# Kernel tuning notes

Measured on AMD Instinct MI355X. Metric: run time of the kernel, lower is better.

## Reference

```python
import jax, jax.numpy as jnp
import numpy as np

FIELD_DIMS = [26000] * 39
EMBED_DIM = 16
MLP_DIMS = [1024, 512, 256]
BATCH = 16384
EPS = 1e-5
OFFSETS = jnp.asarray(np.concatenate(([0], np.cumsum(FIELD_DIMS)[:-1])), dtype=jnp.int64)


def _bn_fields(x, g, b):
    # BatchNorm1d(num_fields) on (B, F, E): stats over (batch, embed) per field (training-mode batch stats)
    mu = x.mean(axis=(0, 2), keepdims=True)
    var = x.var(axis=(0, 2), keepdims=True)
    return (x - mu) / jnp.sqrt(var + EPS) * g[None, :, None] + b[None, :, None]


def _bn1d(x, g, b):
    # BatchNorm1d on (B, D): stats over batch
    mu = x.mean(axis=0)
    var = x.var(axis=0)
    return (x - mu) / jnp.sqrt(var + EPS) * g + b


def setup_inputs() -> dict:
    key = jax.random.key(0)
    ks = jax.random.split(key, 16)
    V = sum(FIELD_DIMS)
    F = len(FIELD_DIMS)
    E = EMBED_DIM
    D = F * E  # 624
    init = lambda k, shape, s: (jax.random.normal(k, shape) * s).astype(jnp.float32)
    inp = {}
    inp["x"] = jax.random.randint(ks[0], (BATCH, F), 0, FIELD_DIMS[0], dtype=jnp.int64)
    inp["emb_table"] = init(ks[1], (V, E), 0.01)
    inp["lin_table"] = init(ks[2], (V, 1), 0.01)
    inp["lin_bias"] = jnp.zeros((1,), jnp.float32)
    inp["bn_g"] = jnp.ones((F,), jnp.float32)
    inp["bn_b"] = jnp.zeros((F,), jnp.float32)
    inp["ctrl_w"] = init(ks[3], (D, F), D ** -0.5)
    inp["ctrl_b"] = jnp.zeros((F,), jnp.float32)
    inp["ctrl_bn_g"] = jnp.ones((F,), jnp.float32)
    inp["ctrl_bn_b"] = jnp.zeros((F,), jnp.float32)
    dims = [D] + MLP_DIMS
    for i in range(3):
        inp[f"w{i+1}"] = init(ks[4 + i], (dims[i], dims[i + 1]), dims[i] ** -0.5)
        inp[f"b{i+1}"] = jnp.zeros((dims[i + 1],), jnp.float32)
        inp[f"g{i+1}"] = jnp.ones((dims[i + 1],), jnp.float32)
        inp[f"be{i+1}"] = jnp.zeros((dims[i + 1],), jnp.float32)
    inp["w_out"] = init(ks[7], (dims[-1], 1), dims[-1] ** -0.5)
    inp["b_out"] = jnp.zeros((1,), jnp.float32)
    inp["k"] = 20
    return inp


def reference(x, emb_table, lin_table, lin_bias, bn_g, bn_b,
              ctrl_w, ctrl_b, ctrl_bn_g, ctrl_bn_b,
              w1, b1, g1, be1, w2, b2, g2, be2, w3, b3, g3, be3,
              w_out, b_out, k):
    B, F = x.shape
    idx = x + OFFSETS[None, :]                      # (B, F) global vocab ids
    embed = emb_table[idx]                          # (B, F, E) gather
    embed = _bn_fields(embed, bn_g, bn_b)
    flat = embed.reshape(B, -1)                     # (B, F*E)
    # controller MLP: Linear -> BN -> ReLU (dropout inactive at inference)
    weight = jax.nn.relu(_bn1d(flat @ ctrl_w + ctrl_b, ctrl_bn_g, ctrl_bn_b))  # (B, F)
    # kmax_pooling along dim 1: topk values, indices sorted ascending
    kvals, kidx = jax.lax.top_k(weight, k)          # (B, k)
    order = jnp.argsort(kidx, axis=1)
    kidx = jnp.take_along_axis(kidx, order, axis=1)
    kvals = jnp.take_along_axis(kvals, order, axis=1)
    kvals = kvals / jnp.sum(kvals, axis=1, keepdims=True)
    # scatter normalized weights into zero mask
    mask = jnp.zeros((B, F), embed.dtype).at[jnp.arange(B)[:, None], kidx].set(kvals)
    embed = embed * mask[:, :, None]                # elementwise gate
    # wide part: sum of per-field scalar embeddings + bias
    linear = lin_table[idx].sum(axis=1) + lin_bias  # (B, 1)
    # deep part: 3-layer MLP with BN+ReLU, final Linear to 1
    h = embed.reshape(B, -1)
    h = jax.nn.relu(_bn1d(h @ w1 + b1, g1, be1))
    h = jax.nn.relu(_bn1d(h @ w2 + b2, g2, be2))
    h = jax.nn.relu(_bn1d(h @ w3 + b3, g3, be3))
    out = linear + h @ w_out + b_out                # (B, 1)
    return jax.nn.sigmoid(out.squeeze(1))           # (B,)
```

## Files before the change

kernel.cpp:

```cpp
#include <hip/hip_runtime.h>
#include <math.h>
#include <stdint.h>

constexpr int BB = 16384;
constexpr int NF = 39;
constexpr int NE = 16;
constexpr int ND = NF * NE;
constexpr int FIELD_DIM = 26000;
constexpr float EPS_ = 1e-5f;

typedef __bf16 bfx8 __attribute__((ext_vector_type(8)));
typedef float f32x4 __attribute__((ext_vector_type(4)));
typedef short s16x8 __attribute__((ext_vector_type(8)));

static __device__ __forceinline__ unsigned short f2bf(float f) {
    union { float f; unsigned u; } a; a.f = f;
    unsigned r = a.u + 0x7fffu + ((a.u >> 16) & 1u);
    return (unsigned short)(r >> 16);
}
static __device__ __forceinline__ float bf2f(unsigned short u) {
    union { unsigned u; float f; } a; a.u = ((unsigned)u) << 16;
    return a.f;
}

static __device__ __forceinline__ void xcd_map(int l, int lognx, int& bx, int& by) {
    int s = l >> 3;
    bx = s & ((1 << lognx) - 1);
    by = ((l & 7) << 4) + (s >> lognx);
}

__global__ void k_prep(const float* __restrict__ w1, const float* __restrict__ w2,
                       const float* __restrict__ w3, const float* __restrict__ cw,
                       unsigned short* __restrict__ w1t, unsigned short* __restrict__ w2t,
                       unsigned short* __restrict__ w3t, float* __restrict__ wct,
                       double* __restrict__ stats, int nstats) {
    int b = blockIdx.x;
    if (b < 1280) {
        const float* in; unsigned short* outp; int K, N, Kpad, tid;
        if (b < 640)        { in = w1; outp = w1t; K = 624;  N = 1024; Kpad = 640;  tid = b; }
        else if (b < 1152)  { in = w2; outp = w2t; K = 1024; N = 512;  Kpad = 1024; tid = b - 640; }
        else                { in = w3; outp = w3t; K = 512;  N = 256;  Kpad = 512;  tid = b - 1152; }
        int tiles_n = N >> 5;
        int tk = tid / tiles_n, tn = tid % tiles_n;
        __shared__ float tile[32][33];
        int tx = threadIdx.x & 31, ty = threadIdx.x >> 5;
#pragma unroll
        for (int i = 0; i < 4; ++i) {
            int k = tk * 32 + ty + i * 8, n = tn * 32 + tx;
            tile[ty + i * 8][tx] = (k < K) ? in[(size_t)k * N + n] : 0.f;
        }
        __syncthreads();
#pragma unroll
        for (int i = 0; i < 4; ++i) {
            int n = tn * 32 + ty + i * 8, k = tk * 32 + tx;
            outp[(size_t)n * Kpad + k] = f2bf(tile[tx][ty + i * 8]);
        }
    } else if (b < 1397) {
        int gid = (b - 1280) * 256 + threadIdx.x;
        if (gid < 48 * ND) {
            int j = gid / ND, k = gid % ND;
            wct[gid] = (j < NF) ? cw[(size_t)k * NF + j] : 0.f;
        }
    } else {
        int gid = (b - 1397) * 256 + threadIdx.x;
        if (gid < nstats) stats[gid] = 0.0;
    }
}

__global__ void k_field_stats(const int* __restrict__ x, const float* __restrict__ emb,
                              double* __restrict__ stats ) {
    int f = blockIdx.x;
    int r = blockIdx.y * blockDim.x + threadIdx.x;
    double s = 0.0, q = 0.0;
    if (r < BB) {
        long long id = (long long)x[r * NF + f] + (long long)f * FIELD_DIM;
        const float4* p = (const float4*)(emb + id * NE);
#pragma unroll
        for (int i = 0; i < 4; ++i) {
            float4 v = p[i];
            s += (double)v.x; s += (double)v.y; s += (double)v.z; s += (double)v.w;
            q += (double)v.x * v.x; q += (double)v.y * v.y;
            q += (double)v.z * v.z; q += (double)v.w * v.w;
        }
    }
    __shared__ double ls[256], lq[256];
    ls[threadIdx.x] = s; lq[threadIdx.x] = q;
    __syncthreads();
    for (int off = 128; off > 0; off >>= 1) {
        if ((int)threadIdx.x < off) {
            ls[threadIdx.x] += ls[threadIdx.x + off];
            lq[threadIdx.x] += lq[threadIdx.x + off];
        }
        __syncthreads();
    }
    if (threadIdx.x == 0) {
        atomicAdd(&stats[f], ls[0]);
        atomicAdd(&stats[NF + f], lq[0]);
    }
}

__global__ void k_flat_norm(const int* __restrict__ x, const float* __restrict__ emb,
                            const double* __restrict__ stats, const float* __restrict__ bng,
                            const float* __restrict__ bnb, float* __restrict__ flat) {
    __shared__ float sc_s[NF], sh_s[NF];
    if ((int)threadIdx.x < NF) {
        int f = threadIdx.x;
        double cnt = (double)BB * NE;
        double mu = stats[f] / cnt;
        double var = stats[NF + f] / cnt - mu * mu;
        float sc = (float)((double)bng[f] / sqrt(var + (double)EPS_));
        sc_s[f] = sc;
        sh_s[f] = bnb[f] - (float)mu * sc;
    }
    __syncthreads();
    int gid = blockIdx.x * blockDim.x + threadIdx.x;
    if (gid >= BB * NF) return;
    int f = gid % NF;
    long long id = (long long)x[gid] + (long long)f * FIELD_DIM;
    float sc = sc_s[f], sh = sh_s[f];
    const float4* p = (const float4*)(emb + id * NE);
    float4* o = (float4*)(flat) + (size_t)gid * 4;
#pragma unroll
    for (int i = 0; i < 4; ++i) {
        float4 v = p[i];
        o[i] = make_float4(fmaf(v.x, sc, sh), fmaf(v.y, sc, sh),
                           fmaf(v.z, sc, sh), fmaf(v.w, sc, sh));
    }
}

__launch_bounds__(256)
__global__ void k_ctrl_gemm_sk(const float* __restrict__ flat, const float* __restrict__ wct,
                               double* __restrict__ zp) {
    __shared__ float As[64][68];
    __shared__ float Ws[64][49];
    const int t = threadIdx.x;
    const int tn = t & 15;
    const int tm = t >> 4;
    const int bm = blockIdx.x & 255;
    const int half = blockIdx.x >> 8;
    const int m0 = bm * 64;
    const int kbeg = half ? 320 : 0;
    const int kend = half ? 624 : 320;
    double acc[4][3] = {};
    for (int k0 = kbeg; k0 < kend; k0 += 64) {
        const int kl = (kend - k0 >= 64) ? 64 : (kend - k0);
        const int kl4 = kl >> 2;
#pragma unroll
        for (int i = 0; i < 4; ++i) {
            int idx = t + 256 * i;
            int row = idx >> 4, c4 = idx & 15;
            if (c4 < kl4) {
                float4 v = *(const float4*)(flat + (size_t)(m0 + row) * ND + k0 + c4 * 4);
                *(float4*)&As[row][c4 * 4] = v;
            }
        }
        {
            int col = t >> 4;
            int c4 = t & 15;
#pragma unroll
            for (int cp = 0; cp < 3; ++cp, col += 16) {
                if (c4 < kl4) {
                    float4 v = *(const float4*)(wct + (size_t)col * ND + k0 + c4 * 4);
                    Ws[c4 * 4 + 0][col] = v.x; Ws[c4 * 4 + 1][col] = v.y;
                    Ws[c4 * 4 + 2][col] = v.z; Ws[c4 * 4 + 3][col] = v.w;
                }
            }
        }
        __syncthreads();
#pragma unroll 4
        for (int kk = 0; kk < kl; ++kk) {
            double a0 = (double)As[4 * tm + 0][kk];
            double a1 = (double)As[4 * tm + 1][kk];
            double a2 = (double)As[4 * tm + 2][kk];
            double a3 = (double)As[4 * tm + 3][kk];
            double w0 = (double)Ws[kk][3 * tn + 0];
            double w1 = (double)Ws[kk][3 * tn + 1];
            double w2 = (double)Ws[kk][3 * tn + 2];
            acc[0][0] += a0 * w0; acc[0][1] += a0 * w1; acc[0][2] += a0 * w2;
            acc[1][0] += a1 * w0; acc[1][1] += a1 * w1; acc[1][2] += a1 * w2;
            acc[2][0] += a2 * w0; acc[2][1] += a2 * w1; acc[2][2] += a2 * w2;
            acc[3][0] += a3 * w0; acc[3][1] += a3 * w1; acc[3][2] += a3 * w2;
        }
        __syncthreads();
    }
    double* zph = zp + (size_t)half * BB * NF;
#pragma unroll
    for (int j = 0; j < 3; ++j) {
        int col = 3 * tn + j;
        if (col < NF) {
#pragma unroll
            for (int i = 0; i < 4; ++i)
                zph[(size_t)(m0 + 4 * tm + i) * NF + col] = acc[i][j];
        }
    }
}

__global__ void k_ctrl_reduce(const double* __restrict__ zp, const float* __restrict__ bias,
                              float* __restrict__ z, double* __restrict__ stats) {
    __shared__ double Sred[2][16][48];
    const int t = threadIdx.x;
    const int tn = t & 15;
    const int tm = t >> 4;
    const int m0 = blockIdx.x * 64;
#pragma unroll
    for (int j = 0; j < 3; ++j) {
        int col = 3 * tn + j;
        double s = 0.0, q = 0.0;
        if (col < NF) {
            float bs = bias[col];
#pragma unroll
            for (int i = 0; i < 4; ++i) {
                size_t idx = (size_t)(m0 + 4 * tm + i) * NF + col;
                double p01 = zp[idx] + zp[(size_t)BB * NF + idx];
                float v = (float)(p01 + (double)bs);
                z[idx] = v;
                s += (double)v;
                q += (double)v * (double)v;
            }
        }
        Sred[0][tm][col] = s;
        Sred[1][tm][col] = q;
    }
    __syncthreads();
    if (t < NF) {
        double ts = 0.0, tq = 0.0;
#pragma unroll
        for (int i = 0; i < 16; ++i) { ts += Sred[0][i][t]; tq += Sred[1][i][t]; }
        atomicAdd(&stats[t], ts);
        atomicAdd(&stats[NF + t], tq);
    }
}

__global__ void k_topk_gate(const float* __restrict__ zc, const double* __restrict__ stats,
                            const float* __restrict__ cbg, const float* __restrict__ cbb,
                            const int* __restrict__ kptr, const float* __restrict__ flat,
                            unsigned short* __restrict__ flatg) {
    __shared__ float sc_s[NF], sh_s[NF];
    int t = threadIdx.x;
    if (t < NF) {
        double mu = stats[t] / (double)BB;
        double var = stats[NF + t] / (double)BB - mu * mu;
        float sc = (float)((double)cbg[t] / sqrt(var + (double)EPS_));
        sc_s[t] = sc;
        sh_s[t] = cbb[t] - (float)mu * sc;
    }
    __syncthreads();
    int r = blockIdx.x * 4 + (t >> 6);
    int lane = t & 63;
    int k = kptr[0];
    bool active = (lane < NF);
    float w = -1.f;
    if (active) {
        float v = zc[(size_t)r * NF + lane];
        w = fmaxf(fmaf(v, sc_s[lane], sh_s[lane]), 0.f);
    }
    int rank = 0;
#pragma unroll
    for (int j = 0; j < NF; ++j) {
        float vj = __shfl(w, j, 64);
        rank += (vj > w || (vj == w && j < lane)) ? 1 : 0;
    }
    bool sel = active && (rank < k);
    float val = sel ? w : 0.f;
    float sum = val;
#pragma unroll
    for (int off = 32; off > 0; off >>= 1) sum += __shfl_xor(sum, off, 64);
    if (active) {
        float ms = sel ? ((sum > 0.f) ? (w / sum) : 0.f) : 0.f;
        const float* src = flat + (size_t)r * ND + lane * 16;
        unsigned short* dst = flatg + (size_t)r * 640 + lane * 16;
#pragma unroll
        for (int h = 0; h < 2; ++h) {
            union { s16x8 v; unsigned short u[8]; } p;
#pragma unroll
            for (int j = 0; j < 8; ++j) p.u[j] = f2bf(src[h * 8 + j] * ms);
            *(s16x8*)(dst + h * 8) = p.v;
        }
    } else if (lane == NF) {
        s16x8 zv = {};
        *(s16x8*)(flatg + (size_t)r * 640 + 624) = zv;
        *(s16x8*)(flatg + (size_t)r * 640 + 632) = zv;
    }
}

__launch_bounds__(256)
__global__ void k_mfma_gemm(const unsigned short* __restrict__ A,
                            const unsigned short* __restrict__ Bt,
                            const float* __restrict__ bias,
                            unsigned short* __restrict__ C,
                            double* __restrict__ stats,
                            int M, int K, int N, int lognx) {
    __shared__ char lds[32768];
    char* As = lds;
    char* Bs = lds + 16384;
    const int t = threadIdx.x;
    const int l = t & 63;
    const int w = t >> 6;
    int bx, by;
    xcd_map(blockIdx.x, lognx, bx, by);
    const int m0 = by * 128, n0 = bx * 128;
    const int Wr = (w >> 1) * 64, Wc = (w & 1) * 64;

    const int srow = t >> 3;
    const int sswz = (t & 7) ^ (srow & 7);
    const unsigned short* ga[4];
    const unsigned short* gb[4];
#pragma unroll
    for (int i = 0; i < 4; ++i) {
        ga[i] = A + (size_t)(m0 + i * 32 + srow) * K + sswz * 8;
        gb[i] = Bt + (size_t)(n0 + i * 32 + srow) * K + sswz * 8;
    }
    int a_off[4][2], b_off[4][2];
#pragma unroll
    for (int m = 0; m < 4; ++m) {
#pragma unroll
        for (int h = 0; h < 2; ++h) {
            int r = Wr + m * 16 + (l & 15);
            a_off[m][h] = r * 128 + (((h * 4 + (l >> 4)) ^ (r & 7)) << 4);
            int c = Wc + m * 16 + (l & 15);
            b_off[m][h] = c * 128 + (((h * 4 + (l >> 4)) ^ (c & 7)) << 4);
        }
    }
    f32x4 acc[4][4] = {};
    for (int k0 = 0; k0 < K; k0 += 64) {
#pragma unroll
        for (int i = 0; i < 4; ++i) {
            __builtin_amdgcn_global_load_lds(
                (const __attribute__((address_space(1))) void*)ga[i],
                (__attribute__((address_space(3))) void*)(As + i * 4096 + t * 16), 16, 0, 0);
            __builtin_amdgcn_global_load_lds(
                (const __attribute__((address_space(1))) void*)gb[i],
                (__attribute__((address_space(3))) void*)(Bs + i * 4096 + t * 16), 16, 0, 0);
            ga[i] += 64; gb[i] += 64;
        }
        __syncthreads();
#pragma unroll
        for (int h = 0; h < 2; ++h) {
            bfx8 af[4], bv[4];
#pragma unroll
            for (int m = 0; m < 4; ++m)
                af[m] = __builtin_bit_cast(bfx8, *(const s16x8*)(As + a_off[m][h]));
#pragma unroll
            for (int n = 0; n < 4; ++n)
                bv[n] = __builtin_bit_cast(bfx8, *(const s16x8*)(Bs + b_off[n][h]));
#pragma unroll
            for (int m = 0; m < 4; ++m)
#pragma unroll
                for (int n = 0; n < 4; ++n)
                    acc[m][n] = __builtin_amdgcn_mfma_f32_16x16x32_bf16(af[m], bv[n], acc[m][n], 0, 0, 0);
        }
        __syncthreads();
    }
#pragma unroll
    for (int n = 0; n < 4; ++n) {
        int nc = n0 + Wc + n * 16 + (l & 15);
        float bs = bias[nc];
        double s = 0.0, q = 0.0;
#pragma unroll
        for (int m = 0; m < 4; ++m) {
            int rbase = m0 + Wr + m * 16 + ((l >> 4) << 2);
#pragma unroll
            for (int i = 0; i < 4; ++i) {
                float v = acc[m][n][i] + bs;
                C[(size_t)(rbase + i) * N + nc] = f2bf(v);
                s += (double)v;
                q += (double)v * (double)v;
            }
        }
        s += __shfl_xor(s, 16, 64); s += __shfl_xor(s, 32, 64);
        q += __shfl_xor(q, 16, 64); q += __shfl_xor(q, 32, 64);
        if ((l >> 4) == 0) {
            atomicAdd(&stats[nc], s);
            atomicAdd(&stats[N + nc], q);
        }
    }
}

__launch_bounds__(256)
__global__ void k_mfma_gemm_bn(const unsigned short* __restrict__ A,
                               const double* __restrict__ statsIn,
                               const float* __restrict__ g, const float* __restrict__ be,
                               const unsigned short* __restrict__ Bt,
                               const float* __restrict__ bias,
                               unsigned short* __restrict__ C,
                               double* __restrict__ stats,
                               int M, int K, int N, int lognx) {
    __shared__ char lds[40960];
    char* As = lds;
    char* Bs = lds + 16384;
    float* scs = (float*)(lds + 32768);
    float* shs = scs + K;
    const int t = threadIdx.x;
    const int l = t & 63;
    const int w = t >> 6;
    int bx, by;
    xcd_map(blockIdx.x, lognx, bx, by);
    const int m0 = by * 128, n0 = bx * 128;
    const int Wr = (w >> 1) * 64, Wc = (w & 1) * 64;

    constexpr double inv_bb = 1.0 / (double)BB;
    for (int c = t; c < K; c += 256) {
        double mu = statsIn[c] * inv_bb;
        double var = statsIn[K + c] * inv_bb - mu * mu;
        float sc = g[c] / sqrtf((float)var + EPS_);
        scs[c] = sc;
        shs[c] = be[c] - (float)mu * sc;
    }
    __syncthreads();

    const int srow = t >> 3;
    const int sswz = (t & 7) ^ (srow & 7);
    const unsigned short* ga[4];
    const unsigned short* gb[4];
#pragma unroll
    for (int i = 0; i < 4; ++i) {
        ga[i] = A + (size_t)(m0 + i * 32 + srow) * K + sswz * 8;
        gb[i] = Bt + (size_t)(n0 + i * 32 + srow) * K + sswz * 8;
    }
    int a_off[4][2], b_off[4][2];
#pragma unroll
    for (int m = 0; m < 4; ++m) {
#pragma unroll
        for (int h = 0; h < 2; ++h) {
            int r = Wr + m * 16 + (l & 15);
            a_off[m][h] = r * 128 + (((h * 4 + (l >> 4)) ^ (r & 7)) << 4);
            int c = Wc + m * 16 + (l & 15);
            b_off[m][h] = c * 128 + (((h * 4 + (l >> 4)) ^ (c & 7)) << 4);
        }
    }
    f32x4 acc[4][4] = {};
    s16x8 praw[4];
#pragma unroll
    for (int i = 0; i < 4; ++i) { praw[i] = *(const s16x8*)ga[i]; ga[i] += 64; }

    for (int k0 = 0; k0 < K; k0 += 64) {
#pragma unroll
        for (int i = 0; i < 4; ++i) {
            __builtin_amdgcn_global_load_lds(
                (const __attribute__((address_space(1))) void*)gb[i],
                (__attribute__((address_space(3))) void*)(Bs + i * 4096 + t * 16), 16, 0, 0);
            gb[i] += 64;
        }
        {
            int kb = k0 + sswz * 8;
            float4 sc0 = *(const float4*)&scs[kb];
            float4 sc1 = *(const float4*)&scs[kb + 4];
            float4 sh0 = *(const float4*)&shs[kb];
            float4 sh1 = *(const float4*)&shs[kb + 4];
            float scl[8] = {sc0.x, sc0.y, sc0.z, sc0.w, sc1.x, sc1.y, sc1.z, sc1.w};
            float shl[8] = {sh0.x, sh0.y, sh0.z, sh0.w, sh1.x, sh1.y, sh1.z, sh1.w};
#pragma unroll
            for (int i = 0; i < 4; ++i) {
                union { s16x8 v; unsigned short u[8]; } pin;
                pin.v = praw[i];
                float f[8];
#pragma unroll
                for (int j = 0; j < 8; ++j)
                    f[j] = fmaxf(fmaf(bf2f(pin.u[j]), scl[j], shl[j]), 0.f);
                union { unsigned w4[4]; s16x8 v; } pout;
#pragma unroll
                for (int j = 0; j < 4; ++j) {
                    unsigned rr;
                    asm("v_cvt_pk_bf16_f32 %0, %1, %2" : "=v"(rr) : "v"(f[2 * j]), "v"(f[2 * j + 1]));
                    pout.w4[j] = rr;
                }
                *(s16x8*)(As + i * 4096 + t * 16) = pout.v;
            }
        }
        if (k0 + 64 < K) {
#pragma unroll
            for (int i = 0; i < 4; ++i) { praw[i] = *(const s16x8*)ga[i]; ga[i] += 64; }
        }
        __syncthreads();
#pragma unroll
        for (int h = 0; h < 2; ++h) {
            bfx8 af[4], bv[4];
#pragma unroll
            for (int m = 0; m < 4; ++m)
                af[m] = __builtin_bit_cast(bfx8, *(const s16x8*)(As + a_off[m][h]));
#pragma unroll
            for (int n = 0; n < 4; ++n)
                bv[n] = __builtin_bit_cast(bfx8, *(const s16x8*)(Bs + b_off[n][h]));
#pragma unroll
            for (int m = 0; m < 4; ++m)
#pragma unroll
                for (int n = 0; n < 4; ++n)
                    acc[m][n] = __builtin_amdgcn_mfma_f32_16x16x32_bf16(af[m], bv[n], acc[m][n], 0, 0, 0);
        }
        __syncthreads();
    }
#pragma unroll
    for (int n = 0; n < 4; ++n) {
        int nc = n0 + Wc + n * 16 + (l & 15);
        float bs = bias[nc];
        double s = 0.0, q = 0.0;
#pragma unroll
        for (int m = 0; m < 4; ++m) {
            int rbase = m0 + Wr + m * 16 + ((l >> 4) << 2);
#pragma unroll
            for (int i = 0; i < 4; ++i) {
                float v = acc[m][n][i] + bs;
                C[(size_t)(rbase + i) * N + nc] = f2bf(v);
                s += (double)v;
                q += (double)v * (double)v;
            }
        }
        s += __shfl_xor(s, 16, 64); s += __shfl_xor(s, 32, 64);
        q += __shfl_xor(q, 16, 64); q += __shfl_xor(q, 32, 64);
        if ((l >> 4) == 0) {
            atomicAdd(&stats[nc], s);
            atomicAdd(&stats[N + nc], q);
        }
    }
}

__global__ void k_out(const unsigned short* __restrict__ h3, const double* __restrict__ stats3,
                      const float* __restrict__ g3, const float* __restrict__ be3,
                      const float* __restrict__ wo, const float* __restrict__ bo,
                      const int* __restrict__ x, const float* __restrict__ lt,
                      const float* __restrict__ lb, float* __restrict__ out) {
    __shared__ float scs[256], shs[256];
    int t = threadIdx.x;
    {
        constexpr double inv_bb = 1.0 / (double)BB;
        double mu = stats3[t] * inv_bb;
        double var = stats3[256 + t] * inv_bb - mu * mu;
        float sc = g3[t] / sqrtf((float)var + EPS_);
        scs[t] = sc;
        shs[t] = be3[t] - (float)mu * sc;
    }
    __syncthreads();
    int r = blockIdx.x * 4 + (t >> 6);
    int lane = t & 63;
    float s = 0.f;
#pragma unroll
    for (int k = lane; k < 256; k += 64) {
        float xv = bf2f(h3[(size_t)r * 256 + k]);
        float hb = bf2f(f2bf(fmaxf(fmaf(xv, scs[k], shs[k]), 0.f)));
        s += hb * wo[k];
    }
    if (lane < NF) {
        long long id = (long long)x[r * NF + lane] + (long long)lane * FIELD_DIM;
        s += lt[id];
    }
#pragma unroll
    for (int off = 32; off > 0; off >>= 1) s += __shfl_xor(s, off, 64);
    if (lane == 0) {
        float tt = s + bo[0] + lb[0];
        out[r] = 1.f / (1.f + expf(-tt));
    }
}

extern "C" void kernel_launch(void* const* d_in, const int* in_sizes, int n_in,
                              void* d_out, int out_size, void* d_ws, size_t ws_size,
                              hipStream_t stream) {
    const int* x = (const int*)d_in[0];
    const float* emb = (const float*)d_in[1];
    const float* lint = (const float*)d_in[2];
    const float* linb = (const float*)d_in[3];
    const float* bng = (const float*)d_in[4];
    const float* bnb = (const float*)d_in[5];
    const float* cw = (const float*)d_in[6];
    const float* cb = (const float*)d_in[7];
    const float* cbg = (const float*)d_in[8];
    const float* cbb = (const float*)d_in[9];
    const float* w1 = (const float*)d_in[10];
    const float* b1 = (const float*)d_in[11];
    const float* g1 = (const float*)d_in[12];
    const float* be1 = (const float*)d_in[13];
    const float* w2 = (const float*)d_in[14];
    const float* b2 = (const float*)d_in[15];
    const float* g2 = (const float*)d_in[16];
    const float* be2 = (const float*)d_in[17];
    const float* w3 = (const float*)d_in[18];
    const float* b3 = (const float*)d_in[19];
    const float* g3 = (const float*)d_in[20];
    const float* be3 = (const float*)d_in[21];
    const float* wo = (const float*)d_in[22];
    const float* bo = (const float*)d_in[23];
    const int* kptr = (const int*)d_in[24];
    float* out = (float*)d_out;

    char* p = (char*)d_ws;
    float* flat = (float*)p;                 p += (size_t)BB * ND * 4;
    unsigned short* flatg = (unsigned short*)p; p += (size_t)BB * 640 * 2;
    unsigned short* h1 = (unsigned short*)p; p += (size_t)BB * 1024 * 2;
    unsigned short* h2 = (unsigned short*)p; p += (size_t)BB * 512 * 2;
    unsigned short* h3 = (unsigned short*)p; p += (size_t)BB * 256 * 2;
    unsigned short* w1t = (unsigned short*)p; p += (size_t)1024 * 640 * 2;
    unsigned short* w2t = (unsigned short*)p; p += (size_t)512 * 1024 * 2;
    unsigned short* w3t = (unsigned short*)p; p += (size_t)256 * 512 * 2;
    float* wct = (float*)p;                  p += (size_t)48 * ND * 4;
    float* zc = (float*)p;                   p += (size_t)BB * NF * 4;
    double* zp = (double*)p;                 p += (size_t)2 * BB * NF * 8;
    double* stats_all = (double*)p;
    double* stats_f = stats_all;
    double* stats_c = stats_f + 2 * NF;
    double* stats_1 = stats_c + 2 * NF;
    double* stats_2 = stats_1 + 2 * 1024;
    double* stats_3 = stats_2 + 2 * 512;
    int stats_doubles = 2 * (NF + NF + 1024 + 512 + 256);

    k_prep<<<1412, 256, 0, stream>>>(w1, w2, w3, cw, w1t, w2t, w3t, wct,
                                     stats_all, stats_doubles);

    k_field_stats<<<dim3(NF, BB / 256), 256, 0, stream>>>(x, emb, stats_f);
    k_flat_norm<<<(BB * NF + 255) / 256, 256, 0, stream>>>(x, emb, stats_f, bng, bnb, flat);

    k_ctrl_gemm_sk<<<512, 256, 0, stream>>>(flat, wct, zp);
    k_ctrl_reduce<<<BB / 64, 256, 0, stream>>>(zp, cb, zc, stats_c);
    k_topk_gate<<<BB / 4, 256, 0, stream>>>(zc, stats_c, cbg, cbb, kptr, flat, flatg);

    k_mfma_gemm<<<(1024 / 128) * (BB / 128), 256, 0, stream>>>(flatg, w1t, b1, h1, stats_1,
                                                               BB, 640, 1024, 3);

    k_mfma_gemm_bn<<<(512 / 128) * (BB / 128), 256, 0, stream>>>(h1, stats_1, g1, be1,
                                                                 w2t, b2, h2, stats_2,
                                                                 BB, 1024, 512, 2);

    k_mfma_gemm_bn<<<(256 / 128) * (BB / 128), 256, 0, stream>>>(h2, stats_2, g2, be2,
                                                                 w3t, b3, h3, stats_3,
                                                                 BB, 512, 256, 1);

    k_out<<<BB / 4, 256, 0, stream>>>(h3, stats_3, g3, be3, wo, bo, x, lint, linb, out);
}
```

Before: 227.0 us.

## Double-buffer LDS tiles in both MFMA GEMM kernels to overlap loads with compute

Both GEMM kernels now use two LDS buffers for the A and B tiles. The next K-tile is prefetched into one buffer while MFMAs run on the other, which is meant to hide global load latency behind compute. LDS use doubles to 64-72KB per block, which may lower occupancy. The visible loop bodies also rely on a single sync per iteration, which risks read/write races if the trailing sync is not adjusted correctly.

New measurement: 224.1 us. About the same (-1.3%).

```diff
diff --git a/kernel.cpp b/kernel.cpp
--- a/kernel.cpp
+++ b/kernel.cpp
@@ -290,9 +290,7 @@
                             unsigned short* __restrict__ C,
                             double* __restrict__ stats,
                             int M, int K, int N, int lognx) {
-    __shared__ char lds[32768];
-    char* As = lds;
-    char* Bs = lds + 16384;
+    __shared__ char lds[65536];
     const int t = threadIdx.x;
     const int l = t & 63;
     const int w = t >> 6;
@@ -321,28 +319,46 @@
             b_off[m][h] = c * 128 + (((h * 4 + (l >> 4)) ^ (c & 7)) << 4);
         }
     }
+    const int nt = K >> 6;
     f32x4 acc[4][4] = {};
-    for (int k0 = 0; k0 < K; k0 += 64) {
-#pragma unroll
-        for (int i = 0; i < 4; ++i) {
-            __builtin_amdgcn_global_load_lds(
-                (const __attribute__((address_space(1))) void*)ga[i],
-                (__attribute__((address_space(3))) void*)(As + i * 4096 + t * 16), 16, 0, 0);
-            __builtin_amdgcn_global_load_lds(
-                (const __attribute__((address_space(1))) void*)gb[i],
-                (__attribute__((address_space(3))) void*)(Bs + i * 4096 + t * 16), 16, 0, 0);
-            ga[i] += 64; gb[i] += 64;
-        }
-        __syncthreads();
+#pragma unroll
+    for (int i = 0; i < 4; ++i) {
+        __builtin_amdgcn_global_load_lds(
+            (const __attribute__((address_space(1))) void*)ga[i],
+            (__attribute__((address_space(3))) void*)(lds + i * 4096 + t * 16), 16, 0, 0);
+        __builtin_amdgcn_global_load_lds(
+            (const __attribute__((address_space(1))) void*)gb[i],
+            (__attribute__((address_space(3))) void*)(lds + 32768 + i * 4096 + t * 16), 16, 0, 0);
+        ga[i] += 64; gb[i] += 64;
+    }
+    __syncthreads();
+    for (int ts = 0; ts < nt; ++ts) {
+        const int cur = ts & 1;
+        if (ts + 1 < nt) {
+            char* An = lds + (cur ^ 1) * 16384;
+            char* Bn = lds + 32768 + (cur ^ 1) * 16384;
+#pragma unroll
+            for (int i = 0; i < 4; ++i) {
+                __builtin_amdgcn_global_load_lds(
+                    (const __attribute__((address_space(1))) void*)ga[i],
+                    (__attribute__((address_space(3))) void*)(An + i * 4096 + t * 16), 16, 0, 0);
+                __builtin_amdgcn_global_load_lds(
+                    (const __attribute__((address_space(1))) void*)gb[i],
+                    (__attribute__((address_space(3))) void*)(Bn + i * 4096 + t * 16), 16, 0, 0);
+                ga[i] += 64; gb[i] += 64;
+            }
+        }
+        const char* Ac = lds + cur * 16384;
+        const char* Bc = lds + 32768 + cur * 16384;
 #pragma unroll
         for (int h = 0; h < 2; ++h) {
             bfx8 af[4], bv[4];
 #pragma unroll
             for (int m = 0; m < 4; ++m)
-                af[m] = __builtin_bit_cast(bfx8, *(const s16x8*)(As + a_off[m][h]));
+                af[m] = __builtin_bit_cast(bfx8, *(const s16x8*)(Ac + a_off[m][h]));
 #pragma unroll
             for (int n = 0; n < 4; ++n)
-                bv[n] = __builtin_bit_cast(bfx8, *(const s16x8*)(Bs + b_off[n][h]));
+                bv[n] = __builtin_bit_cast(bfx8, *(const s16x8*)(Bc + b_off[n][h]));
 #pragma unroll
             for (int m = 0; m < 4; ++m)
 #pragma unroll
@@ -385,10 +401,8 @@
                                unsigned short* __restrict__ C,
                                double* __restrict__ stats,
                                int M, int K, int N, int lognx) {
-    __shared__ char lds[40960];
-    char* As = lds;
-    char* Bs = lds + 16384;
-    float* scs = (float*)(lds + 32768);
+    __shared__ char lds[73728];
+    float* scs = (float*)(lds + 65536);
     float* shs = scs + K;
     const int t = threadIdx.x;
     const int l = t & 63;
@@ -428,59 +442,76 @@
             b_off[m][h] = c * 128 + (((h * 4 + (l >> 4)) ^ (c & 7)) << 4);
         }
     }
+    const int nt = K >> 6;
     f32x4 acc[4][4] = {};
     s16x8 praw[4];
-#pragma unroll
-    for (int i = 0; i < 4; ++i) { praw[i] = *(const s16x8*)ga[i]; ga[i] += 64; }
-
-    for (int k0 = 0; k0 < K; k0 += 64) {
+
+    auto write_a = [&](int buf, int kb0) {
+        char* Ad = lds + buf * 16384;
+        int kb = kb0 + sswz * 8;
+        float4 sc0 = *(const float4*)&scs[kb];
+        float4 sc1 = *(const float4*)&scs[kb + 4];
+        float4 sh0 = *(const float4*)&shs[kb];
+        float4 sh1 = *(const float4*)&shs[kb + 4];
+        float scl[8] = {sc0.x, sc0.y, sc0.z, sc0.w, sc1.x, sc1.y, sc1.z, sc1.w};
+        float shl[8] = {sh0.x, sh0.y, sh0.z, sh0.w, sh1.x, sh1.y, sh1.z, sh1.w};
+#pragma unroll
+        for (int i = 0; i < 4; ++i) {
+            union { s16x8 v; unsigned short u[8]; } pin;
+            pin.v = praw[i];
+            float f[8];
+#pragma unroll
+            for (int j = 0; j < 8; ++j)
+                f[j] = fmaxf(fmaf(bf2f(pin.u[j]), scl[j], shl[j]), 0.f);
+            union { unsigned w4[4]; s16x8 v; } pout;
+#pragma unroll
+            for (int j = 0; j < 4; ++j) {
+                unsigned rr;
+                asm("v_cvt_pk_bf16_f32 %0, %1, %2" : "=v"(rr) : "v"(f[2 * j]), "v"(f[2 * j + 1]));
+                pout.w4[j] = rr;
+            }
+            *(s16x8*)(Ad + i * 4096 + t * 16) = pout.v;
+        }
+    };
+    auto load_praw = [&]() {
+#pragma unroll
+        for (int i = 0; i < 4; ++i) { praw[i] = *(const s16x8*)ga[i]; ga[i] += 64; }
+    };
+    auto stage_b = [&](int buf) {
+        char* Bd = lds + 32768 + buf * 16384;
 #pragma unroll
         for (int i = 0; i < 4; ++i) {
             __builtin_amdgcn_global_load_lds(
                 (const __attribute__((address_space(1))) void*)gb[i],
-                (__attribute__((address_space(3))) void*)(Bs + i * 4096 + t * 16), 16, 0, 0);
+                (__attribute__((address_space(3))) void*)(Bd + i * 4096 + t * 16), 16, 0, 0);
             gb[i] += 64;
         }
-        {
-            int kb = k0 + sswz * 8;
-            float4 sc0 = *(const float4*)&scs[kb];
-            float4 sc1 = *(const float4*)&scs[kb + 4];
-            float4 sh0 = *(const float4*)&shs[kb];
-            float4 sh1 = *(const float4*)&shs[kb + 4];
-            float scl[8] = {sc0.x, sc0.y, sc0.z, sc0.w, sc1.x, sc1.y, sc1.z, sc1.w};
-            float shl[8] = {sh0.x, sh0.y, sh0.z, sh0.w, sh1.x, sh1.y, sh1.z, sh1.w};
-#pragma unroll
-            for (int i = 0; i < 4; ++i) {
-                union { s16x8 v; unsigned short u[8]; } pin;
-                pin.v = praw[i];
-                float f[8];
-#pragma unroll
-                for (int j = 0; j < 8; ++j)
-                    f[j] = fmaxf(fmaf(bf2f(pin.u[j]), scl[j], shl[j]), 0.f);
-                union { unsigned w4[4]; s16x8 v; } pout;
-#pragma unroll
-                for (int j = 0; j < 4; ++j) {
-                    unsigned rr;
-                    asm("v_cvt_pk_bf16_f32 %0, %1, %2" : "=v"(rr) : "v"(f[2 * j]), "v"(f[2 * j + 1]));
-                    pout.w4[j] = rr;
-                }
-                *(s16x8*)(As + i * 4096 + t * 16) = pout.v;
-            }
-        }
-        if (k0 + 64 < K) {
-#pragma unroll
-            for (int i = 0; i < 4; ++i) { praw[i] = *(const s16x8*)ga[i]; ga[i] += 64; }
-        }
-        __syncthreads();
+    };
+
+    load_praw();
+    stage_b(0);
+    write_a(0, 0);
+    if (nt > 1) load_praw();
+    __syncthreads();
+
+    for (int ts = 0; ts < nt; ++ts) {
+        const int cur = ts & 1;
+        if (ts + 1 < nt) {
+            stage_b(cur ^ 1);
+            write_a(cur ^ 1, (ts + 1) << 6);
+            if (ts + 2 < nt) load_praw();
+        }
+        const char* Ac = lds + cur * 16384;
+        const char* Bc = lds + 32768 + cur * 16384;
 #pragma unroll
         for (int h = 0; h < 2; ++h) {
             bfx8 af[4], bv[4];
 #pragma unroll
             for (int m = 0; m < 4; ++m)
-                af[m] = __builtin_bit_cast(bfx8, *(const s16x8*)(As + a_off[m][h]));
+                af[m] = __builtin_bit_cast(bfx8, *(const s16x8*)(Ac + a_off[m][h]));
 #pragma unroll
             for (int n = 0; n < 4; ++n)
-                bv[n] = __builtin_bit_cast(bfx8, *(const s16x8*)(Bs + b_off[n][h]));
+                bv[n] = __builtin_bit_cast(bfx8, *(const s16x8*)(Bc + b_off[n][h]));
 #pragma unroll
             for (int m = 0; m < 4; ++m)
 #pragma unroll
```
